# Kernel optimization log

Hardware: AMD Instinct MI355X
Metric: run time of the kernel (lower is better)

## Reference

```python
import jax, jax.numpy as jnp
import numpy as np

N, B, E, H, L, NF = 32768, 2048, 524288, 128, 7, 10
NODE_F = 60  # 10 frames * (loc 3 + vel 3)
OUT_F = 30   # 10 frames * 3


def _mlp(x, W1, b1, W2, b2):
    return jax.nn.relu(x @ W1 + b1) @ W2 + b2


def _lin(key, fan_in, fan_out):
    s = 1.0 / np.sqrt(fan_in)
    kw, kb = jax.random.split(key)
    W = jax.random.uniform(kw, (fan_in, fan_out), jnp.float32, -s, s)
    b = jax.random.uniform(kb, (fan_out,), jnp.float32, -s, s)
    return W, b


def setup_inputs() -> dict:
    key = jax.random.key(0)
    ks = jax.random.split(key, 12)
    p = {}
    p["loc"] = jax.random.normal(ks[0], (N, NF, 3), jnp.float32)
    p["vel"] = jax.random.normal(ks[1], (N, NF, 3), jnp.float32)
    p["y"] = jax.random.normal(ks[2], (N, NF, 3), jnp.float32)
    p["edge_index"] = jax.random.randint(ks[3], (2, E), 0, N, dtype=jnp.int64)
    p["batch_size"] = B
    # embedder: Linear(60,H) -> ReLU -> Linear(H,H)
    p["emb_W1"], p["emb_b1"] = _lin(ks[4], NODE_F, H)
    p["emb_W2"], p["emb_b2"] = _lin(ks[5], H, H)
    # per-layer message net Linear(2H,H)->ReLU->Linear(H,H); update net Linear(2H,H)->ReLU->Linear(H,H)
    mW1, mb1, mW2, mb2, uW1, ub1, uW2, ub2 = [], [], [], [], [], [], [], []
    for i in range(L):
        k = jax.random.fold_in(ks[6], i)
        k1, k2, k3, k4 = jax.random.split(k, 4)
        a, b = _lin(k1, 2 * H, H); mW1.append(a); mb1.append(b)
        a, b = _lin(k2, H, H); mW2.append(a); mb2.append(b)
        a, b = _lin(k3, 2 * H, H); uW1.append(a); ub1.append(b)
        a, b = _lin(k4, H, H); uW2.append(a); ub2.append(b)
    p["msg_W1"] = jnp.stack(mW1); p["msg_b1"] = jnp.stack(mb1)
    p["msg_W2"] = jnp.stack(mW2); p["msg_b2"] = jnp.stack(mb2)
    p["upd_W1"] = jnp.stack(uW1); p["upd_b1"] = jnp.stack(ub1)
    p["upd_W2"] = jnp.stack(uW2); p["upd_b2"] = jnp.stack(ub2)
    # head: Linear(H,H) -> ReLU -> Linear(H,30)
    p["head_W1"], p["head_b1"] = _lin(ks[7], H, H)
    p["head_W2"], p["head_b2"] = _lin(ks[8], H, OUT_F)
    return p


def reference(loc, vel, y, edge_index, batch_size,
              emb_W1, emb_b1, emb_W2, emb_b2,
              msg_W1, msg_b1, msg_W2, msg_b2,
              upd_W1, upd_b1, upd_W2, upd_b2,
              head_W1, head_b1, head_W2, head_b2):
    n = loc.shape[0]
    src, dst = edge_index[0], edge_index[1]  # x_j = x[src], x_i = x[dst] (PyG source_to_target)
    x = jnp.concatenate([loc, vel], axis=-1).reshape(n, -1)  # (N, 60)
    x = _mlp(x, emb_W1, emb_b1, emb_W2, emb_b2)              # (N, H)
    for i in range(L):
        m_in = jnp.concatenate([x[dst], x[src]], axis=-1)    # (E, 2H) cat(x_i, x_j)
        msg = _mlp(m_in, msg_W1[i], msg_b1[i], msg_W2[i], msg_b2[i])  # (E, H)
        agg = jax.ops.segment_sum(msg, dst, num_segments=n)  # scatter-add at targets
        x = _mlp(jnp.concatenate([x, agg], axis=-1), upd_W1[i], upd_b1[i], upd_W2[i], upd_b2[i])
    x = _mlp(x, head_W1, head_b1, head_W2, head_b2)          # (N, 30)
    loc_pred = x.reshape(n, NF, 3) + loc
    d = jnp.sqrt(jnp.sum((loc_pred - y) ** 2, axis=-1))      # (N, NF)
    ade_loss = d.reshape(batch_size, -1, NF).mean(axis=-1).mean(axis=-1)  # (B,)
    fde = jnp.sqrt(jnp.sum((loc_pred[:, -1, :] - y[:, -1, :]) ** 2, axis=-1))  # (N,)
    fde_loss = fde.reshape(batch_size, -1).mean(axis=-1)     # (B,)
    backprop_loss = ade_loss.mean()
    return backprop_loss, ade_loss, fde_loss
```

## Files before the change

### kernel.cpp

```cpp
#include <hip/hip_runtime.h>
#include <hip/hip_bf16.h>
#include <stdint.h>

#define HH 128

typedef __attribute__((ext_vector_type(8))) short short8;
typedef __attribute__((ext_vector_type(4))) float floatx4;

typedef __attribute__((address_space(3))) uint32_t lds_u32_t;
typedef const __attribute__((address_space(1))) uint32_t gbl_u32_t;

__device__ __forceinline__ void gl_lds16(const void* g, void* l) {
  __builtin_amdgcn_global_load_lds((gbl_u32_t*)g, (lds_u32_t*)l, 16, 0, 0);
}

__device__ __forceinline__ float bf2f(short v) {
  union { uint32_t u; float f; } x; x.u = ((uint32_t)(uint16_t)v) << 16; return x.f;
}
__device__ __forceinline__ short f2bf(float f) {
  union { float f; uint32_t u; } x; x.f = f;
  uint32_t r = x.u + 0x7fffu + ((x.u >> 16) & 1u);
  return (short)(r >> 16);
}
__device__ __forceinline__ float rdf(const void* p, int i, int fl) {
  return fl ? bf2f(((const short*)p)[i]) : ((const float*)p)[i];
}


__global__ void detect_zero(const int* __restrict__ eidx, int* iflag, int* dflag,
                            int* __restrict__ counts, float* accp,
                            const uint32_t* __restrict__ loc, int N) {
  int g = blockIdx.x * 256 + threadIdx.x;
  if (g < N) counts[g] = 0;
  if (blockIdx.x == 0) {
    __shared__ int nz, cnt;
    if (threadIdx.x == 0) { nz = 0; cnt = 0; *accp = 0.f; }
    __syncthreads();
    int any = 0;
    for (int i = threadIdx.x; i < 1024; i += 256) any |= (eidx[2 * i + 1] != 0);
    if (any) atomicOr(&nz, 1);
    uint32_t u = loc[threadIdx.x];
    int e = (u >> 7) & 0xFF;
    if (e >= 100 && e <= 140) atomicAdd(&cnt, 1);
    __syncthreads();
    if (threadIdx.x == 0) {
      *iflag = (nz == 0) ? 1 : 0;
      *dflag = (cnt >= 192) ? 1 : 0;
    }
  }
}


__global__ void pad_input(const void* __restrict__ loc, const void* __restrict__ vel,
                          short* __restrict__ dst, const int* __restrict__ dflag) {
  int fl = *dflag;
  int idx = blockIdx.x * 256 + threadIdx.x;
  int j = idx & 63, i = idx >> 6;
  short v = 0;
  if (j < 60) {
    int f = j / 6, c = j % 6;
    float x = (c < 3) ? rdf(loc, (i * 10 + f) * 3 + c, fl)
                      : rdf(vel, (i * 10 + f) * 3 + (c - 3), fl);
    v = f2bf(x);
  }
  dst[idx] = v;
}

struct WPrep {
  const void* src[8];
// ... 97 lines not shown
  int x = c;
#pragma unroll
  for (int off = 1; off < 64; off <<= 1) {
    int u = __shfl_up(x, off);
    if (lane >= off) x += u;
  }
  if (lane == 63) wsum[w] = x;
  __syncthreads();
  int wpre = 0;
#pragma unroll
  for (int k = 0; k < 4; ++k)
    if (k < w) wpre += wsum[k];
  int excl = shb[0] + shb[1] + wpre + x - c;
  if (i < N) {
    row_start[i] = excl;
    cursor[i] = excl;
    deg[i] = (float)c;
  }
  if (i == N - 1) row_start[N] = E;
}

__global__ void scatter_kernel(const int* __restrict__ eidx, const int* __restrict__ iflag,
                               int* __restrict__ cursor, int* __restrict__ ssrc, int E) {
  int e = blockIdx.x * 256 + threadIdx.x;
  if (e >= E) return;
  int fl = *iflag;
  int d = fl ? eidx[2 * (E + e)] : eidx[E + e];
  int sv = fl ? eidx[2 * e] : eidx[e];
  int pos = atomicAdd(&cursor[d], 1);
  ssrc[pos] = sv;
}


__global__ __launch_bounds__(256)
void edge_agg(const uint32_t* __restrict__ Pp, const uint32_t* __restrict__ Qp,
              const int* __restrict__ ssrc, const int* __restrict__ row_start,
              uint32_t* __restrict__ Hagg, int Ntot) {
  int w = threadIdx.x >> 6, lane = threadIdx.x & 63;
  int d = blockIdx.x * 4 + w;
  if (d >= Ntot) return;
  uint32_t pv = Pp[(size_t)d * 64 + lane];
  float px = bf2f((short)(pv & 0xffff));
  float py = bf2f((short)(pv >> 16));
  int s0 = row_start[d], s1 = row_start[d + 1];
  float ax = 0.f, ay = 0.f;
  int e = s0;
  for (; e + 8 <= s1; e += 8) {
    int idx[8];
    uint32_t q[8];
#pragma unroll
    for (int u = 0; u < 8; ++u) idx[u] = ssrc[e + u];
#pragma unroll
    for (int u = 0; u < 8; ++u) q[u] = Qp[(size_t)idx[u] * 64 + lane];
#pragma unroll
    for (int u = 0; u < 8; ++u) {
      float hx = px + bf2f((short)(q[u] & 0xffff));
      float hy = py + bf2f((short)(q[u] >> 16));
      ax += hx > 0.f ? hx : 0.f;
      ay += hy > 0.f ? hy : 0.f;
    }
  }
  for (; e < s1; ++e) {
    int i0 = ssrc[e];
    uint32_t q0 = Qp[(size_t)i0 * 64 + lane];
    float hx = px + bf2f((short)(q0 & 0xffff));
    float hy = py + bf2f((short)(q0 >> 16));
    ax += hx > 0.f ? hx : 0.f;
    ay += hy > 0.f ? hy : 0.f;
  }
  uint32_t packed = (uint32_t)(uint16_t)f2bf(ax) | ((uint32_t)(uint16_t)f2bf(ay) << 16);
  Hagg[(size_t)d * 64 + lane] = packed;
}


__device__ __forceinline__ void write_aslots_q(char* lds, const floatx4 v[2][4],
                                               int wr, int wc, int quad, int l16) {
#pragma unroll
  for (int mt = 0; mt < 2; ++mt) {
    int g = wr * 2 + mt;
#pragma unroll
    for (int nt = 0; nt < 4; ++nt) {
      int s2 = wc * 2 + (nt >> 1);
      int qc = (nt & 1) * 2 + (l16 >> 3);
      char* base = lds + (size_t)(s2 * 8 + g) * 1024 + 2 * (l16 & 7);
#pragma unroll
      for (int r = 0; r < 4; ++r)
        *(short*)(base + (quad * 4 + r + 16 * qc) * 16) = f2bf(v[mt][nt][r]);
    }
  }
}

template <int NT, int TS>
__device__ __forceinline__ void gemm_q(const char* lds, int wr, int wc,
                                       floatx4 acc[2][NT], int lane) {
#pragma unroll
  for (int s2 = 0; s2 < 4; ++s2) {
    short8 af[2];
#pragma unroll
    for (int mt = 0; mt < 2; ++mt)
      af[mt] = *(const short8*)(lds + (s2 * 8 + wr * 2 + mt) * 1024 + lane * 16);
    short8 bf[NT];
#pragma unroll
    for (int nt = 0; nt < NT; ++nt)
      bf[nt] = *(const short8*)(lds + 32768 + (s2 * TS + wc * NT + nt) * 1024 + lane * 16);
#pragma unroll
    for (int mt = 0; mt < 2; ++mt)
#pragma unroll
      for (int nt = 0; nt < NT; ++nt)
        acc[mt][nt] = __builtin_amdgcn_mfma_f32_16x16x32_bf16(af[mt], bf[nt], acc[mt][nt], 0, 0, 0);
  }
}


template <int MODE>
__global__ __launch_bounds__(512, 2)
void mlp_fused(const short* __restrict__ Asrc, const short* __restrict__ Asrc2,
               const short* __restrict__ W1T, const float* __restrict__ b1,
               const short* __restrict__ W2T, const float* __restrict__ b2,
               const float* __restrict__ deg, const float* __restrict__ b2Uv,
               const short* __restrict__ pqW1, const float* __restrict__ pqB1,
               const short* __restrict__ pq2W, const float* __restrict__ pq2B,
               short* __restrict__ xout, short* __restrict__ Pout,
               short* __restrict__ Qout, float* __restrict__ out32) {
  constexpr int K1 = (MODE == 0) ? 64 : 256;
  constexpr int NS = K1 / 32;
  constexpr int PQS = (MODE == 3) ? 128 : 256;

  __shared__ __align__(16) char lds[65536];

  const int tid = threadIdx.x;
  const int w = tid >> 6, lane = tid & 63;
  const int quad = lane >> 4, l16 = lane & 15;
  const int wr = w >> 1, wc = w & 1;
  const int R0 = blockIdx.x * 128;
  const int CB = wc * 64;

#pragma unroll
  for (int c = 0; c < NS; ++c) {
    int slot = w * NS + c;
    int s = slot >> 3, t = slot & 7;
    int n = t * 16 + l16, k = s * 32 + quad * 8;
    gl_lds16(W1T + n * K1 + k, lds + slot * 1024 + lane * 16);
  }

  short8 afrag[NS][2];
  if constexpr (MODE == 0) {
#pragma unroll
    for (int mt = 0; mt < 2; ++mt) {
      int m = R0 + wr * 32 + mt * 16 + l16;
      const short* pr = Asrc + (size_t)m * 64;
#pragma unroll
      for (int s = 0; s < NS; ++s) afrag[s][mt] = *(const short8*)(pr + s * 32 + quad * 8);
    }
  } else {
#pragma unroll
    for (int mt = 0; mt < 2; ++mt) {
      int m = R0 + wr * 32 + mt * 16 + l16;
      const short* pr = Asrc + (size_t)m * HH;
      const short* ar = Asrc2 + (size_t)m * HH;
#pragma unroll
      for (int s = 0; s < 4; ++s) {
        afrag[s][mt] = *(const short8*)(pr + s * 32 + quad * 8);
        afrag[s + 4][mt] = *(const short8*)(ar + s * 32 + quad * 8);
      }
    }
  }

  float b1f[4], b2f[4], pb1[4], b2u[4];
  float dvals[2][4];
#pragma unroll
  for (int t = 0; t < 4; ++t) {
    int col = CB + t * 16 + l16;
    b1f[t] = b1[col];
    b2f[t] = b2[col];
    pb1[t] = pqB1[col];
  }
  if constexpr (MODE != 0) {
#pragma unroll
    for (int t = 0; t < 4; ++t) b2u[t] = b2Uv[CB + t * 16 + l16];
#pragma unroll
    for (int mt = 0; mt < 2; ++mt)
#pragma unroll
      for (int r = 0; r < 4; ++r)
        dvals[mt][r] = deg[R0 + wr * 32 + mt * 16 + quad * 4 + r];
  }

  __syncthreads();

  floatx4 zero4 = {0.f, 0.f, 0.f, 0.f};
  floatx4 acc[2][4];
#pragma unroll
  for (int mt = 0; mt < 2; ++mt)
#pragma unroll
    for (int t = 0; t < 4; ++t) acc[mt][t] = zero4;
#pragma unroll
  for (int s = 0; s < NS; ++s) {
    short8 bfrag[4];
#pragma unroll
    for (int nt = 0; nt < 4; ++nt)
      bfrag[nt] = *(const short8*)(lds + (s * 8 + wc * 4 + nt) * 1024 + lane * 16);
#pragma unroll
    for (int mt = 0; mt < 2; ++mt)
#pragma unroll
      for (int nt = 0; nt < 4; ++nt)
        acc[mt][nt] = __builtin_amdgcn_mfma_f32_16x16x32_bf16(afrag[s][mt], bfrag[nt], acc[mt][nt], 0, 0, 0);
  }

  __syncthreads();

#pragma unroll
  for (int c = 0; c < 4; ++c) {
    int slot = w * 4 + c;
    int s2 = slot >> 3, t = slot & 7;
    int n = t * 16 + l16, k = s2 * 32 + quad * 8;
    gl_lds16(W2T + n * HH + k, lds + 32768 + slot * 1024 + lane * 16);
  }
  {
    floatx4 hv[2][4];
#pragma unroll
    for (int mt = 0; mt < 2; ++mt)
#pragma unroll
      for (int nt = 0; nt < 4; ++nt)
#pragma unroll
        for (int r = 0; r < 4; ++r) {
          float h = acc[mt][nt][r] + b1f[nt];
          if constexpr (MODE != 0) h += dvals[mt][r] * b2u[nt];
          hv[mt][nt][r] = h > 0.f ? h : 0.f;
        }
    write_aslots_q(lds, hv, wr, wc, quad, l16);
  }

  __syncthreads();

  floatx4 acc2[2][4];
#pragma unroll
  for (int mt = 0; mt < 2; ++mt)
#pragma unroll
    for (int t = 0; t < 4; ++t) acc2[mt][t] = zero4;
  gemm_q<4, 8>(lds, wr, wc, acc2, lane);

  floatx4 xv[2][4];
#pragma unroll
  for (int mt = 0; mt < 2; ++mt)
#pragma unroll
    for (int nt = 0; nt < 4; ++nt)
#pragma unroll
      for (int r = 0; r < 4; ++r)
        xv[mt][nt][r] = acc2[mt][nt][r] + b2f[nt];

  if constexpr (MODE != 3) {
#pragma unroll
    for (int mt = 0; mt < 2; ++mt)
#pragma unroll
      for (int nt = 0; nt < 4; ++nt) {
        int col = CB + nt * 16 + l16;
#pragma unroll
        for (int r = 0; r < 4; ++r) {
          int row = R0 + wr * 32 + mt * 16 + quad * 4 + r;
          xout[(size_t)row * HH + col] = f2bf(xv[mt][nt][r]);
        }
      }
  }

  __syncthreads();

  write_aslots_q(lds, xv, wr, wc, quad, l16);
#pragma unroll
  for (int c = 0; c < 4; ++c) {
    int slot = w * 4 + c;
    int s2 = slot >> 3, t = slot & 7;
    int n = t * 16 + l16, k = s2 * 32 + quad * 8;
    gl_lds16(pqW1 + n * PQS + k, lds + 32768 + slot * 1024 + lane * 16);
  }

  __syncthreads();

  floatx4 accc[2][4];
#pragma unroll
  for (int mt = 0; mt < 2; ++mt)
#pragma unroll
    for (int t = 0; t < 4; ++t) accc[mt][t] = zero4;
  gemm_q<4, 8>(lds, wr, wc, accc, lane);

  if constexpr (MODE == 3) {
    floatx4 h2[2][4];
#pragma unroll
    for (int mt = 0; mt < 2; ++mt)
#pragma unroll
      for (int nt = 0; nt < 4; ++nt)
#pragma unroll
        for (int r = 0; r < 4; ++r) {
          float h = accc[mt][nt][r] + pb1[nt];
          h2[mt][nt][r] = h > 0.f ? h : 0.f;
        }
    __syncthreads();
    write_aslots_q(lds, h2, wr, wc, quad, l16);
    {
      int s2 = w >> 1, t = w & 1;
      int n = t * 16 + l16, k = s2 * 32 + quad * 8;
      gl_lds16(pq2W + n * 128 + k, lds + 32768 + w * 1024 + lane * 16);
    }
    __syncthreads();
    floatx4 acco[2][1];
#pragma unroll
    for (int mt = 0; mt < 2; ++mt) acco[mt][0] = zero4;
    gemm_q<1, 2>(lds, wr, wc, acco, lane);
    float ob = pq2B[wc * 16 + l16];
#pragma unroll
    for (int mt = 0; mt < 2; ++mt) {
      int col = wc * 16 + l16;
#pragma unroll
      for (int r = 0; r < 4; ++r) {
        int row = R0 + wr * 32 + mt * 16 + quad * 4 + r;
        out32[(size_t)row * 32 + col] = acco[mt][0][r] + ob;
      }
    }
  } else {
#pragma unroll
    for (int mt = 0; mt < 2; ++mt)
#pragma unroll
      for (int nt = 0; nt < 4; ++nt) {
        int col = CB + nt * 16 + l16;
#pragma unroll
        for (int r = 0; r < 4; ++r) {
          int row = R0 + wr * 32 + mt * 16 + quad * 4 + r;
          Pout[(size_t)row * HH + col] = f2bf(accc[mt][nt][r] + pb1[nt]);
        }
      }
    __syncthreads();
#pragma unroll
    for (int c = 0; c < 4; ++c) {
      int slot = w * 4 + c;
      int s2 = slot >> 3, t = slot & 7;
      int n = t * 16 + l16, k = s2 * 32 + quad * 8;
      gl_lds16(pqW1 + n * 256 + 128 + k, lds + 32768 + slot * 1024 + lane * 16);
    }
    __syncthreads();
    floatx4 accq[2][4];
#pragma unroll
    for (int mt = 0; mt < 2; ++mt)
#pragma unroll
      for (int t = 0; t < 4; ++t) accq[mt][t] = zero4;
    gemm_q<4, 8>(lds, wr, wc, accq, lane);
#pragma unroll
    for (int mt = 0; mt < 2; ++mt)
#pragma unroll
      for (int nt = 0; nt < 4; ++nt) {
        int col = CB + nt * 16 + l16;
#pragma unroll
        for (int r = 0; r < 4; ++r) {
          int row = R0 + wr * 32 + mt * 16 + quad * 4 + r;
          Qout[(size_t)row * HH + col] = f2bf(accq[mt][nt][r]);
        }
      }
  }
}


__global__ void loss_kernel(const float* __restrict__ out32, const void* __restrict__ loc,
                            const void* __restrict__ yv, const int* __restrict__ dflag,
                            float* __restrict__ out, float* __restrict__ acc, int NB) {
  int fl = *dflag;
  int i = blockIdx.x * 256 + threadIdx.x;
  const float* o = out32 + (size_t)i * 32;
  float dsum = 0.f, fde = 0.f;
#pragma unroll
  for (int f = 0; f < 10; ++f) {
    float dx = o[f * 3 + 0] + rdf(loc, i * 30 + f * 3 + 0, fl) - rdf(yv, i * 30 + f * 3 + 0, fl);
    float dy = o[f * 3 + 1] + rdf(loc, i * 30 + f * 3 + 1, fl) - rdf(yv, i * 30 + f * 3 + 1, fl);
    float dz = o[f * 3 + 2] + rdf(loc, i * 30 + f * 3 + 2, fl) - rdf(yv, i * 30 + f * 3 + 2, fl);
    float d = sqrtf(dx * dx + dy * dy + dz * dz);
    dsum += d;
    if (f == 9) fde = d;
  }
#pragma unroll
  for (int m = 1; m < 16; m <<= 1) {
    dsum += __shfl_xor(dsum, m);
    fde += __shfl_xor(fde, m);
  }
  if ((threadIdx.x & 15) == 0) {
    int b = i >> 4;
    out[1 + b] = dsum / 160.0f;
    out[1 + NB + b] = fde / 16.0f;
    unsafeAtomicAdd(acc, dsum);
  }
}

__global__ void final_kernel(const float* __restrict__ acc, float* __restrict__ out, float inv) {
  if (threadIdx.x == 0) out[0] = *acc * inv;
}


extern "C" void kernel_launch(void* const* d_in, const int* in_sizes, int n_in,
                              void* d_out, int out_size, void* d_ws, size_t ws_size,
                              hipStream_t stream) {
  const void* loc = d_in[0];
  const void* vel = d_in[1];
  const void* yv = d_in[2];
  const int* eidx = (const int*)d_in[3];

  const int N = in_sizes[0] / 30;
  const int E = in_sizes[3] / 2;
  const int L = 7;
  const int NB = N / 16;

  const size_t MB = 1024 * 1024;
  char* ws = (char*)d_ws;
  short* x = (short*)ws;
  short* P = (short*)(ws + 8 * MB);
  short* Qs = (short*)(ws + 24 * MB);
  short* Hagg = (short*)(ws + 32 * MB);
  short* updW1Tf = (short*)(ws + 40 * MB);
  int* bsums = (int*)(ws + 41 * MB);
  short* wbase = (short*)(ws + 48 * MB);
  const unsigned long long OFF_EMBW1 = 0;
  const unsigned long long OFF_EMBW2 = 8192;
  const unsigned long long OFF_HEADW1 = 24576;
  const unsigned long long OFF_HEADW2 = 40960;
  const unsigned long long OFF_MSGW1 = 45056;
  const unsigned long long OFF_MSGW2 = 274432;
  const unsigned long long OFF_UPDW1 = 389120;
  const unsigned long long OFF_UPDW2 = 618496;
  short* embW1T = wbase + OFF_EMBW1;
  short* embW2T = wbase + OFF_EMBW2;
  short* headW1T = wbase + OFF_HEADW1;
  short* headW2T = wbase + OFF_HEADW2;
  short* msgW1T = wbase + OFF_MSGW1;
  short* msgW2T = wbase + OFF_MSGW2;
  short* updW1T = wbase + OFF_UPDW1;
  short* updW2T = wbase + OFF_UPDW2;
  float* bias = (float*)(ws + 49 * MB + 512 * 1024);
  float* embB1f = bias;
  float* embB2f = bias + 128;
  float* msgB1f = bias + 256;
  float* msgB2f = bias + 1152;
  float* updB1f = bias + 2048;
  float* updB2f = bias + 2944;
  float* headB1f = bias + 3840;
  float* headB2f = bias + 3968;
  float* b2U = bias + 4096;
  int* counts = (int*)(ws + 49 * MB + 768 * 1024);
  int* row_start = (int*)(ws + 50 * MB);
  int* cursor = (int*)(ws + 50 * MB + 256 * 1024);
  float* deg = (float*)(ws + 50 * MB + 512 * 1024);
  int* iflag = (int*)(ws + 50 * MB + 768 * 1024);
  int* dflag = iflag + 16;
  float* accp = (float*)(iflag + 32);
  int* ssrc = (int*)(ws + 51 * MB);
  short* in64 = (short*)(ws + 53 * MB);
  float* out32 = (float*)(ws + 57 * MB);

  const int NBLK = (N + 255) / 256;

  detect_zero<<<NBLK, 256, 0, stream>>>(eidx, iflag, dflag, counts, accp,
                                        (const uint32_t*)loc, N);
  hist_kernel<<<(E + 255) / 256, 256, 0, stream>>>(eidx, iflag, counts, E);
  scan_bsum<<<NBLK, 256, 0, stream>>>(counts, bsums, N);
  scan_final<<<NBLK, 256, 0, stream>>>(counts, bsums, row_start, cursor, deg, N, E);
  scatter_kernel<<<(E + 255) / 256, 256, 0, stream>>>(eidx, iflag, cursor, ssrc, E);

  pad_input<<<(N * 64) / 256, 256, 0, stream>>>(loc, vel, in64, dflag);

  {
    WPrep a;
    const void* srcs[8] = {d_in[5], d_in[7], d_in[17], d_in[19],
                           d_in[9], d_in[11], d_in[13], d_in[15]};
    unsigned long long offs[8] = {OFF_EMBW1, OFF_EMBW2, OFF_HEADW1, OFF_HEADW2,
                                  OFF_MSGW1, OFF_MSGW2, OFF_UPDW1, OFF_UPDW2};
    int Ls[8] = {1, 1, 1, 1, 7, 7, 7, 7};
    int Ks[8] = {60, 128, 128, 128, 256, 128, 256, 128};
    int Ns[8] = {128, 128, 128, 30, 128, 128, 128, 128};
    int Kps[8] = {64, 128, 128, 128, 256, 128, 256, 128};
    int Nps[8] = {128, 128, 128, 32, 128, 128, 128, 128};
    int cum = 0;
    for (int s = 0; s < 8; ++s) {
      a.src[s] = srcs[s]; a.dstoff[s] = offs[s];
      a.L[s] = Ls[s]; a.K[s] = Ks[s]; a.Nn[s] = Ns[s]; a.Kp[s] = Kps[s]; a.Np[s] = Nps[s];
      a.bstart[s] = cum;
      cum += (Ls[s] * Nps[s] * Kps[s] + 255) / 256;
    }
    a.bstart[8] = cum;
    prep_w<<<cum, 256, 0, stream>>>(a, wbase, dflag);
  }
  {
    BPrep a;
    const void* srcs[8] = {d_in[6], d_in[8], d_in[10], d_in[12],
                           d_in[14], d_in[16], d_in[18], d_in[20]};
    int ns[8] = {128, 128, 896, 896, 896, 896, 128, 30};
    int es[9] = {0, 128, 256, 1152, 2048, 2944, 3840, 3968, 4000};
    for (int s = 0; s < 8; ++s) { a.src[s] = srcs[s]; a.n[s] = ns[s]; a.estart[s] = es[s]; }
    a.estart[8] = es[8];
    prep_b<<<16, 256, 0, stream>>>(a, bias, dflag);
  }

  fold_kernel<<<900, 256, 0, stream>>>(updW1T, msgW2T, updW1Tf, msgB2f, b2U);

  mlp_fused<0><<<N / 128, 512, 0, stream>>>(in64, nullptr,
      embW1T, embB1f, embW2T, embB2f, nullptr, nullptr,
      msgW1T, msgB1f, nullptr, nullptr, x, P, Qs, nullptr);

  for (int l = 0; l < L; ++l) {
    edge_agg<<<(N + 3) / 4, 256, 0, stream>>>((const uint32_t*)P, (const uint32_t*)Qs,
                                              ssrc, row_start, (uint32_t*)Hagg, N);
    if (l < L - 1) {
      mlp_fused<2><<<N / 128, 512, 0, stream>>>(x, Hagg,
          updW1Tf + l * 128 * 256, updB1f + l * 128, updW2T + l * 128 * 128, updB2f + l * 128,
          deg, b2U + l * 128,
          msgW1T + (l + 1) * 128 * 256, msgB1f + (l + 1) * 128, nullptr, nullptr,
          x, P, Qs, nullptr);
    } else {
      mlp_fused<3><<<N / 128, 512, 0, stream>>>(x, Hagg,
          updW1Tf + l * 128 * 256, updB1f + l * 128, updW2T + l * 128 * 128, updB2f + l * 128,
          deg, b2U + l * 128,
          headW1T, headB1f, headW2T, headB2f,
          nullptr, nullptr, nullptr, out32);
    }
  }

  loss_kernel<<<N / 256, 256, 0, stream>>>(out32, loc, yv, dflag, (float*)d_out, accp, NB);
  final_kernel<<<1, 64, 0, stream>>>(accp, (float*)d_out, 1.0f / 327680.0f);
}
```

Baseline: 531.4 us.

## Shrink fused MLP tiles to 32 rows with 2 waves and unroll edge tail

The fused node MLP kernel now processes 32 rows per block with 128 threads (2 waves) instead of 128 rows with 512 threads. This launches 4x more blocks and uses a smaller 40KB LDS footprint, so more blocks can be resident and the grid fills the device more evenly. In exchange, each block reloads the full weight matrices, and the K=256 first layer is split into two staged halves, which adds syncs and weight traffic per row. Separately, the edge aggregation remainder loop is replaced by 4/2/1 unrolled tails so more gathers are in flight at once.

```diff
diff --git a/kernel.cpp b/kernel.cpp
--- a/kernel.cpp
+++ b/kernel.cpp
@@ -212,8 +212,7 @@
   float ax = 0.f, ay = 0.f;
   int e = s0;
   for (; e + 8 <= s1; e += 8) {
-    int idx[8];
-    uint32_t q[8];
+    int idx[8]; uint32_t q[8];
 #pragma unroll
     for (int u = 0; u < 8; ++u) idx[u] = ssrc[e + u];
 #pragma unroll
@@ -226,7 +225,32 @@
       ay += hy > 0.f ? hy : 0.f;
     }
   }
-  for (; e < s1; ++e) {
+  if (e + 4 <= s1) {
+    int idx[4]; uint32_t q[4];
+#pragma unroll
+    for (int u = 0; u < 4; ++u) idx[u] = ssrc[e + u];
+#pragma unroll
+    for (int u = 0; u < 4; ++u) q[u] = Qp[(size_t)idx[u] * 64 + lane];
+#pragma unroll
+    for (int u = 0; u < 4; ++u) {
+      float hx = px + bf2f((short)(q[u] & 0xffff));
+      float hy = py + bf2f((short)(q[u] >> 16));
+      ax += hx > 0.f ? hx : 0.f;
+      ay += hy > 0.f ? hy : 0.f;
+    }
+    e += 4;
+  }
+  if (e + 2 <= s1) {
+    int i0 = ssrc[e], i1 = ssrc[e + 1];
+    uint32_t q0 = Qp[(size_t)i0 * 64 + lane];
+    uint32_t q1 = Qp[(size_t)i1 * 64 + lane];
+    float hx = px + bf2f((short)(q0 & 0xffff)), hy = py + bf2f((short)(q0 >> 16));
+    ax += hx > 0.f ? hx : 0.f; ay += hy > 0.f ? hy : 0.f;
+    hx = px + bf2f((short)(q1 & 0xffff)); hy = py + bf2f((short)(q1 >> 16));
+    ax += hx > 0.f ? hx : 0.f; ay += hy > 0.f ? hy : 0.f;
+    e += 2;
+  }
+  if (e < s1) {
     int i0 = ssrc[e];
     uint32_t q0 = Qp[(size_t)i0 * 64 + lane];
     float hx = px + bf2f((short)(q0 & 0xffff));
@@ -239,36 +263,34 @@
 }
 
 
-__device__ __forceinline__ void write_aslots_q(char* lds, const floatx4 v[2][4],
-                                               int wr, int wc, int quad, int l16) {
-#pragma unroll
-  for (int mt = 0; mt < 2; ++mt) {
-    int g = wr * 2 + mt;
+__device__ __forceinline__ void write_aslots32(char* lds, const floatx4 v[2][4],
+                                               int wc, int quad, int l16) {
+#pragma unroll
+  for (int mt = 0; mt < 2; ++mt)
 #pragma unroll
     for (int nt = 0; nt < 4; ++nt) {
       int s2 = wc * 2 + (nt >> 1);
       int qc = (nt & 1) * 2 + (l16 >> 3);
-      char* base = lds + (size_t)(s2 * 8 + g) * 1024 + 2 * (l16 & 7);
+      char* base = lds + (size_t)(s2 * 2 + mt) * 1024 + 2 * (l16 & 7);
 #pragma unroll
       for (int r = 0; r < 4; ++r)
         *(short*)(base + (quad * 4 + r + 16 * qc) * 16) = f2bf(v[mt][nt][r]);
     }
-  }
 }
 
 template <int NT, int TS>
-__device__ __forceinline__ void gemm_q(const char* lds, int wr, int wc,
-                                       floatx4 acc[2][NT], int lane) {
+__device__ __forceinline__ void gemm32(const char* lds, int wc, floatx4 acc[2][NT], int lane) {
+  const char* ldsB = lds + 8192;
 #pragma unroll
   for (int s2 = 0; s2 < 4; ++s2) {
     short8 af[2];
 #pragma unroll
     for (int mt = 0; mt < 2; ++mt)
-      af[mt] = *(const short8*)(lds + (s2 * 8 + wr * 2 + mt) * 1024 + lane * 16);
+      af[mt] = *(const short8*)(lds + (s2 * 2 + mt) * 1024 + lane * 16);
     short8 bf[NT];
 #pragma unroll
     for (int nt = 0; nt < NT; ++nt)
-      bf[nt] = *(const short8*)(lds + 32768 + (s2 * TS + wc * NT + nt) * 1024 + lane * 16);
+      bf[nt] = *(const short8*)(ldsB + (s2 * TS + wc * NT + nt) * 1024 + lane * 16);
 #pragma unroll
     for (int mt = 0; mt < 2; ++mt)
 #pragma unroll
@@ -279,7 +301,7 @@
 
 
 template <int MODE>
-__global__ __launch_bounds__(512, 2)
+__global__ __launch_bounds__(128, 2)
 void mlp_fused(const short* __restrict__ Asrc, const short* __restrict__ Asrc2,
                const short* __restrict__ W1T, const float* __restrict__ b1,
                const short* __restrict__ W2T, const float* __restrict__ b2,
@@ -289,39 +311,49 @@
                short* __restrict__ xout, short* __restrict__ Pout,
                short* __restrict__ Qout, float* __restrict__ out32) {
   constexpr int K1 = (MODE == 0) ? 64 : 256;
-  constexpr int NS = K1 / 32;
+  constexpr int NSA = K1 / 32;
   constexpr int PQS = (MODE == 3) ? 128 : 256;
 
-  __shared__ __align__(16) char lds[65536];
+  __shared__ __align__(16) char lds[40960];
+  char* ldsB = lds + 8192;
 
   const int tid = threadIdx.x;
-  const int w = tid >> 6, lane = tid & 63;
+  const int wc = tid >> 6, lane = tid & 63;
   const int quad = lane >> 4, l16 = lane & 15;
-  const int wr = w >> 1, wc = w & 1;
-  const int R0 = blockIdx.x * 128;
+  const int R0 = blockIdx.x * 32;
   const int CB = wc * 64;
 
-#pragma unroll
-  for (int c = 0; c < NS; ++c) {
-    int slot = w * NS + c;
-    int s = slot >> 3, t = slot & 7;
-    int n = t * 16 + l16, k = s * 32 + quad * 8;
-    gl_lds16(W1T + n * K1 + k, lds + slot * 1024 + lane * 16);
-  }
-
-  short8 afrag[NS][2];
   if constexpr (MODE == 0) {
 #pragma unroll
+    for (int c = 0; c < 8; ++c) {
+      int slot = wc * 8 + c;
+      int s = slot >> 3, t = slot & 7;
+      gl_lds16(W1T + (t * 16 + l16) * 64 + s * 32 + quad * 8,
+               ldsB + slot * 1024 + lane * 16);
+    }
+  } else {
+#pragma unroll
+    for (int c = 0; c < 16; ++c) {
+      int slot = wc * 16 + c;
+      int s2 = slot >> 3, t = slot & 7;
+      gl_lds16(W1T + (t * 16 + l16) * 256 + s2 * 32 + quad * 8,
+               ldsB + slot * 1024 + lane * 16);
+    }
+  }
+
+  short8 afrag[NSA][2];
+  if constexpr (MODE == 0) {
+#pragma unroll
     for (int mt = 0; mt < 2; ++mt) {
-      int m = R0 + wr * 32 + mt * 16 + l16;
+      int m = R0 + mt * 16 + l16;
       const short* pr = Asrc + (size_t)m * 64;
 #pragma unroll
-      for (int s = 0; s < NS; ++s) afrag[s][mt] = *(const short8*)(pr + s * 32 + quad * 8);
+      for (int s = 0; s < 2; ++s) afrag[s][mt] = *(const short8*)(pr + s * 32 + quad * 8);
     }
   } else {
 #pragma unroll
     for (int mt = 0; mt < 2; ++mt) {
-      int m = R0 + wr * 32 + mt * 16 + l16;
+      int m = R0 + mt * 16 + l16;
       const short* pr = Asrc + (size_t)m * HH;
       const short* ar = Asrc2 + (size_t)m * HH;
 #pragma unroll
@@ -348,7 +380,7 @@
     for (int mt = 0; mt < 2; ++mt)
 #pragma unroll
       for (int r = 0; r < 4; ++r)
-        dvals[mt][r] = deg[R0 + wr * 32 + mt * 16 + quad * 4 + r];
+        dvals[mt][r] = deg[R0 + mt * 16 + quad * 4 + r];
   }
 
   __syncthreads();
@@ -359,27 +391,54 @@
   for (int mt = 0; mt < 2; ++mt)
 #pragma unroll
     for (int t = 0; t < 4; ++t) acc[mt][t] = zero4;
-#pragma unroll
-  for (int s = 0; s < NS; ++s) {
-    short8 bfrag[4];
-#pragma unroll
-    for (int nt = 0; nt < 4; ++nt)
-      bfrag[nt] = *(const short8*)(lds + (s * 8 + wc * 4 + nt) * 1024 + lane * 16);
-#pragma unroll
-    for (int mt = 0; mt < 2; ++mt)
+  {
+    constexpr int NS0 = (MODE == 0) ? 2 : 4;
+#pragma unroll
+    for (int s = 0; s < NS0; ++s) {
+      short8 bfrag[4];
 #pragma unroll
       for (int nt = 0; nt < 4; ++nt)
-        acc[mt][nt] = __builtin_amdgcn_mfma_f32_16x16x32_bf16(afrag[s][mt], bfrag[nt], acc[mt][nt], 0, 0, 0);
+        bfrag[nt] = *(const short8*)(ldsB + (s * 8 + wc * 4 + nt) * 1024 + lane * 16);
+#pragma unroll
+      for (int mt = 0; mt < 2; ++mt)
+#pragma unroll
+        for (int nt = 0; nt < 4; ++nt)
+          acc[mt][nt] = __builtin_amdgcn_mfma_f32_16x16x32_bf16(afrag[s][mt], bfrag[nt], acc[mt][nt], 0, 0, 0);
+    }
+  }
+
+  if constexpr (MODE != 0) {
+    __syncthreads();
+#pragma unroll
+    for (int c = 0; c < 16; ++c) {
+      int slot = wc * 16 + c;
+      int s2 = slot >> 3, t = slot & 7;
+      gl_lds16(W1T + (t * 16 + l16) * 256 + 128 + s2 * 32 + quad * 8,
+               ldsB + slot * 1024 + lane * 16);
+    }
+    __syncthreads();
+#pragma unroll
+    for (int s = 0; s < 4; ++s) {
+      short8 bfrag[4];
+#pragma unroll
+      for (int nt = 0; nt < 4; ++nt)
+        bfrag[nt] = *(const short8*)(ldsB + (s * 8 + wc * 4 + nt) * 1024 + lane * 16);
+#pragma unroll
+      for (int mt = 0; mt < 2; ++mt)
+#pragma unroll
+        for (int nt = 0; nt < 4; ++nt)
+          acc[mt][nt] = __builtin_amdgcn_mfma_f32_16x16x32_bf16(afrag[4 + s][mt], bfrag[nt], acc[mt][nt], 0, 0, 0);
+    }
   }
 
   __syncthreads();
 
 #pragma unroll
-  for (int c = 0; c < 4; ++c) {
-    int slot = w * 4 + c;
+  for (int c = 0; c < 16; ++c) {
+    int slot = wc * 16 + c;
     int s2 = slot >> 3, t = slot & 7;
-    int n = t * 16 + l16, k = s2 * 32 + quad * 8;
-    gl_lds16(W2T + n * HH + k, lds + 32768 + slot * 1024 + lane * 16);
+    gl_lds16(W2T + (t * 16 + l16) * HH + s2 * 32 + quad * 8,
+             ldsB + slot * 1024 + lane * 16);
   }
   {
     floatx4 hv[2][4];
@@ -393,7 +452,7 @@
           if constexpr (MODE != 0) h += dvals[mt][r] * b2u[nt];
           hv[mt][nt][r] = h > 0.f ? h : 0.f;
         }
-    write_aslots_q(lds, hv, wr, wc, quad, l16);
+    write_aslots32(lds, hv, wc, quad, l16);
   }
 
   __syncthreads();
@@ -403,7 +462,7 @@
   for (int mt = 0; mt < 2; ++mt)
 #pragma unroll
     for (int t = 0; t < 4; ++t) acc2[mt][t] = zero4;
-  gemm_q<4, 8>(lds, wr, wc, acc2, lane);
+  gemm32<4, 8>(lds, wc, acc2, lane);
 
   floatx4 xv[2][4];
 #pragma unroll
@@ -422,7 +481,7 @@
         int col = CB + nt * 16 + l16;
 #pragma unroll
         for (int r = 0; r < 4; ++r) {
-          int row = R0 + wr * 32 + mt * 16 + quad * 4 + r;
+          int row = R0 + mt * 16 + quad * 4 + r;
           xout[(size_t)row * HH + col] = f2bf(xv[mt][nt][r]);
         }
       }
@@ -430,13 +489,13 @@
 
   __syncthreads();
 
-  write_aslots_q(lds, xv, wr, wc, quad, l16);
-#pragma unroll
-  for (int c = 0; c < 4; ++c) {
-    int slot = w * 4 + c;
+  write_aslots32(lds, xv, wc, quad, l16);
+#pragma unroll
+  for (int c = 0; c < 16; ++c) {
+    int slot = wc * 16 + c;
     int s2 = slot >> 3, t = slot & 7;
-    int n = t * 16 + l16, k = s2 * 32 + quad * 8;
-    gl_lds16(pqW1 + n * PQS + k, lds + 32768 + slot * 1024 + lane * 16);
+    gl_lds16(pqW1 + (t * 16 + l16) * PQS + s2 * 32 + quad * 8,
+             ldsB + slot * 1024 + lane * 16);
   }
 
   __syncthreads();
@@ -446,7 +505,7 @@
   for (int mt = 0; mt < 2; ++mt)
 #pragma unroll
     for (int t = 0; t < 4; ++t) accc[mt][t] = zero4;
-  gemm_q<4, 8>(lds, wr, wc, accc, lane);
+  gemm32<4, 8>(lds, wc, accc, lane);
 
   if constexpr (MODE == 3) {
     floatx4 h2[2][4];
@@ -460,24 +519,26 @@
           h2[mt][nt][r] = h > 0.f ? h : 0.f;
         }
     __syncthreads();
-    write_aslots_q(lds, h2, wr, wc, quad, l16);
-    {
-      int s2 = w >> 1, t = w & 1;
-      int n = t * 16 + l16, k = s2 * 32 + quad * 8;
-      gl_lds16(pq2W + n * 128 + k, lds + 32768 + w * 1024 + lane * 16);
+    write_aslots32(lds, h2, wc, quad, l16);
+#pragma unroll
+    for (int c = 0; c < 4; ++c) {
+      int slot = wc * 4 + c;
+      int s2 = slot >> 1, t = slot & 1;
+      gl_lds16(pq2W + (t * 16 + l16) * 128 + s2 * 32 + quad * 8,
+               ldsB + slot * 1024 + lane * 16);
     }
     __syncthreads();
     floatx4 acco[2][1];
 #pragma unroll
     for (int mt = 0; mt < 2; ++mt) acco[mt][0] = zero4;
-    gemm_q<1, 2>(lds, wr, wc, acco, lane);
+    gemm32<1, 2>(lds, wc, acco, lane);
     float ob = pq2B[wc * 16 + l16];
 #pragma unroll
     for (int mt = 0; mt < 2; ++mt) {
       int col = wc * 16 + l16;
 #pragma unroll
       for (int r = 0; r < 4; ++r) {
-        int row = R0 + wr * 32 + mt * 16 + quad * 4 + r;
+        int row = R0 + mt * 16 + quad * 4 + r;
         out32[(size_t)row * 32 + col] = acco[mt][0][r] + ob;
       }
     }
@@ -489,17 +550,17 @@
         int col = CB + nt * 16 + l16;
 #pragma unroll
         for (int r = 0; r < 4; ++r) {
-          int row = R0 + wr * 32 + mt * 16 + quad * 4 + r;
+          int row = R0 + mt * 16 + quad * 4 + r;
           Pout[(size_t)row * HH + col] = f2bf(accc[mt][nt][r] + pb1[nt]);
         }
       }
     __syncthreads();
 #pragma unroll
-    for (int c = 0; c < 4; ++c) {
-      int slot = w * 4 + c;
+    for (int c = 0; c < 16; ++c) {
+      int slot = wc * 16 + c;
       int s2 = slot >> 3, t = slot & 7;
-      int n = t * 16 + l16, k = s2 * 32 + quad * 8;
-      gl_lds16(pqW1 + n * 256 + 128 + k, lds + 32768 + slot * 1024 + lane * 16);
+      gl_lds16(pqW1 + (t * 16 + l16) * 256 + 128 + s2 * 32 + quad * 8,
+               ldsB + slot * 1024 + lane * 16);
     }
     __syncthreads();
     floatx4 accq[2][4];
@@ -507,7 +568,7 @@
     for (int mt = 0; mt < 2; ++mt)
 #pragma unroll
       for (int t = 0; t < 4; ++t) accq[mt][t] = zero4;
-    gemm_q<4, 8>(lds, wr, wc, accq, lane);
+    gemm32<4, 8>(lds, wc, accq, lane);
 #pragma unroll
     for (int mt = 0; mt < 2; ++mt)
 #pragma unroll
@@ -515,7 +576,7 @@
         int col = CB + nt * 16 + l16;
 #pragma unroll
         for (int r = 0; r < 4; ++r) {
-          int row = R0 + wr * 32 + mt * 16 + quad * 4 + r;
+          int row = R0 + mt * 16 + quad * 4 + r;
           Qout[(size_t)row * HH + col] = f2bf(accq[mt][nt][r]);
         }
       }
@@ -661,7 +722,7 @@
 
   fold_kernel<<<900, 256, 0, stream>>>(updW1T, msgW2T, updW1Tf, msgB2f, b2U);
 
-  mlp_fused<0><<<N / 128, 512, 0, stream>>>(in64, nullptr,
+  mlp_fused<0><<<N / 32, 128, 0, stream>>>(in64, nullptr,
       embW1T, embB1f, embW2T, embB2f, nullptr, nullptr,
       msgW1T, msgB1f, nullptr, nullptr, x, P, Qs, nullptr);
 
@@ -669,13 +730,13 @@
     edge_agg<<<(N + 3) / 4, 256, 0, stream>>>((const uint32_t*)P, (const uint32_t*)Qs,
                                               ssrc, row_start, (uint32_t*)Hagg, N);
     if (l < L - 1) {
-      mlp_fused<2><<<N / 128, 512, 0, stream>>>(x, Hagg,
+      mlp_fused<2><<<N / 32, 128, 0, stream>>>(x, Hagg,
           updW1Tf + l * 128 * 256, updB1f + l * 128, updW2T + l * 128 * 128, updB2f + l * 128,
           deg, b2U + l * 128,
           msgW1T + (l + 1) * 128 * 256, msgB1f + (l + 1) * 128, nullptr, nullptr,
           x, P, Qs, nullptr);
     } else {
-      mlp_fused<3><<<N / 128, 512, 0, stream>>>(x, Hagg,
+      mlp_fused<3><<<N / 32, 128, 0, stream>>>(x, Hagg,
           updW1Tf + l * 128 * 256, updB1f + l * 128, updW2T + l * 128 * 128, updB2f + l * 128,
           deg, b2U + l * 128,
           headW1T, headB1f, headW2T, headB2f,
```

After: 567.8 us. +6.8%, slower.

## Fuse edge aggregation gather into update MLP kernel and drop final kernel

Applied to the files above, without the earlier changes.

Edge aggregation (gather of Q rows by CSR plus ReLU-sum) now runs inside the update MLP kernel and writes the aggregate straight into swizzled LDS, so the Hagg round trip through global memory and one launch per layer go away. P/Q are double-buffered because the same kernel reads the previous layer's values and writes the next layer's. The final scalar reduction is folded into the loss kernel with a last-block ticket counter. The cost is that the irregular gather now runs inside a kernel with 512-thread blocks at 2 blocks per CU, so it may hide gather latency less well than the dedicated kernel did.

```diff
diff --git a/kernel.cpp b/kernel.cpp
--- a/kernel.cpp
+++ b/kernel.cpp
@@ -28,13 +28,13 @@
 
 
 __global__ void detect_zero(const int* __restrict__ eidx, int* iflag, int* dflag,
-                            int* __restrict__ counts, float* accp,
+                            int* __restrict__ counts, float* accp, int* ticket,
                             const uint32_t* __restrict__ loc, int N) {
   int g = blockIdx.x * 256 + threadIdx.x;
   if (g < N) counts[g] = 0;
   if (blockIdx.x == 0) {
     __shared__ int nz, cnt;
-    if (threadIdx.x == 0) { nz = 0; cnt = 0; *accp = 0.f; }
+    if (threadIdx.x == 0) { nz = 0; cnt = 0; *accp = 0.f; *ticket = 0; }
     __syncthreads();
     int any = 0;
     for (int i = threadIdx.x; i < 1024; i += 256) any |= (eidx[2 * i + 1] != 0);
@@ -198,47 +198,6 @@
 }
 
 
-__global__ __launch_bounds__(256)
-void edge_agg(const uint32_t* __restrict__ Pp, const uint32_t* __restrict__ Qp,
-              const int* __restrict__ ssrc, const int* __restrict__ row_start,
-              uint32_t* __restrict__ Hagg, int Ntot) {
-  int w = threadIdx.x >> 6, lane = threadIdx.x & 63;
-  int d = blockIdx.x * 4 + w;
-  if (d >= Ntot) return;
-  uint32_t pv = Pp[(size_t)d * 64 + lane];
-  float px = bf2f((short)(pv & 0xffff));
-  float py = bf2f((short)(pv >> 16));
-  int s0 = row_start[d], s1 = row_start[d + 1];
-  float ax = 0.f, ay = 0.f;
-  int e = s0;
-  for (; e + 8 <= s1; e += 8) {
-    int idx[8];
-    uint32_t q[8];
-#pragma unroll
-    for (int u = 0; u < 8; ++u) idx[u] = ssrc[e + u];
-#pragma unroll
-    for (int u = 0; u < 8; ++u) q[u] = Qp[(size_t)idx[u] * 64 + lane];
-#pragma unroll
-    for (int u = 0; u < 8; ++u) {
-      float hx = px + bf2f((short)(q[u] & 0xffff));
-      float hy = py + bf2f((short)(q[u] >> 16));
-      ax += hx > 0.f ? hx : 0.f;
-      ay += hy > 0.f ? hy : 0.f;
-    }
-  }
-  for (; e < s1; ++e) {
-    int i0 = ssrc[e];
-    uint32_t q0 = Qp[(size_t)i0 * 64 + lane];
-    float hx = px + bf2f((short)(q0 & 0xffff));
-    float hy = py + bf2f((short)(q0 >> 16));
-    ax += hx > 0.f ? hx : 0.f;
-    ay += hy > 0.f ? hy : 0.f;
-  }
-  uint32_t packed = (uint32_t)(uint16_t)f2bf(ax) | ((uint32_t)(uint16_t)f2bf(ay) << 16);
-  Hagg[(size_t)d * 64 + lane] = packed;
-}
-
-
 __device__ __forceinline__ void write_aslots_q(char* lds, const floatx4 v[2][4],
                                                int wr, int wc, int quad, int l16) {
 #pragma unroll
@@ -280,7 +239,9 @@
 
 template <int MODE>
 __global__ __launch_bounds__(512, 2)
-void mlp_fused(const short* __restrict__ Asrc, const short* __restrict__ Asrc2,
+void mlp_fused(const short* __restrict__ Asrc,
+               const uint32_t* __restrict__ Pp, const uint32_t* __restrict__ Qp,
+               const int* __restrict__ ssrc, const int* __restrict__ row_start,
                const short* __restrict__ W1T, const float* __restrict__ b1,
                const short* __restrict__ W2T, const float* __restrict__ b2,
                const float* __restrict__ deg, const float* __restrict__ b2Uv,
@@ -288,11 +249,10 @@
                const short* __restrict__ pq2W, const float* __restrict__ pq2B,
                short* __restrict__ xout, short* __restrict__ Pout,
                short* __restrict__ Qout, float* __restrict__ out32) {
-  constexpr int K1 = (MODE == 0) ? 64 : 256;
-  constexpr int NS = K1 / 32;
   constexpr int PQS = (MODE == 3) ? 128 : 256;
 
   __shared__ __align__(16) char lds[65536];
+  char* HB = lds + 32768;
 
   const int tid = threadIdx.x;
   const int w = tid >> 6, lane = tid & 63;
@@ -301,37 +261,6 @@
   const int R0 = blockIdx.x * 128;
   const int CB = wc * 64;
 
-#pragma unroll
-  for (int c = 0; c < NS; ++c) {
-    int slot = w * NS + c;
-    int s = slot >> 3, t = slot & 7;
-    int n = t * 16 + l16, k = s * 32 + quad * 8;
-    gl_lds16(W1T + n * K1 + k, lds + slot * 1024 + lane * 16);
-  }
-
-  short8 afrag[NS][2];
-  if constexpr (MODE == 0) {
-#pragma unroll
-    for (int mt = 0; mt < 2; ++mt) {
-      int m = R0 + wr * 32 + mt * 16 + l16;
-      const short* pr = Asrc + (size_t)m * 64;
-#pragma unroll
-      for (int s = 0; s < NS; ++s) afrag[s][mt] = *(const short8*)(pr + s * 32 + quad * 8);
-    }
-  } else {
-#pragma unroll
-    for (int mt = 0; mt < 2; ++mt) {
-      int m = R0 + wr * 32 + mt * 16 + l16;
-      const short* pr = Asrc + (size_t)m * HH;
-      const short* ar = Asrc2 + (size_t)m * HH;
-#pragma unroll
-      for (int s = 0; s < 4; ++s) {
-        afrag[s][mt] = *(const short8*)(pr + s * 32 + quad * 8);
-        afrag[s + 4][mt] = *(const short8*)(ar + s * 32 + quad * 8);
-      }
-    }
-  }
-
   float b1f[4], b2f[4], pb1[4], b2u[4];
   float dvals[2][4];
 #pragma unroll
@@ -341,7 +270,66 @@
     b2f[t] = b2[col];
     pb1[t] = pqB1[col];
   }
-  if constexpr (MODE != 0) {
+
+  short8 afrag[4][2];
+  floatx4 zero4 = {0.f, 0.f, 0.f, 0.f};
+  floatx4 acc[2][4];
+#pragma unroll
+  for (int mt = 0; mt < 2; ++mt)
+#pragma unroll
+    for (int t = 0; t < 4; ++t) acc[mt][t] = zero4;
+
+  if constexpr (MODE == 0) {
+#pragma unroll
+    for (int c = 0; c < 2; ++c) {
+      int slot = w * 2 + c;
+      int s = slot >> 3, t = slot & 7;
+      gl_lds16(W1T + (t * 16 + l16) * 64 + s * 32 + quad * 8,
+               lds + slot * 1024 + lane * 16);
+    }
+#pragma unroll
+    for (int mt = 0; mt < 2; ++mt) {
+      int m = R0 + wr * 32 + mt * 16 + l16;
+      const short* pr = Asrc + (size_t)m * 64;
+#pragma unroll
+      for (int s = 0; s < 2; ++s) afrag[s][mt] = *(const short8*)(pr + s * 32 + quad * 8);
+    }
+    __syncthreads();
+#pragma unroll
+    for (int s = 0; s < 2; ++s) {
+      short8 bfrag[4];
+#pragma unroll
+      for (int nt = 0; nt < 4; ++nt)
+        bfrag[nt] = *(const short8*)(lds + (s * 8 + wc * 4 + nt) * 1024 + lane * 16);
+#pragma unroll
+      for (int mt = 0; mt < 2; ++mt)
+#pragma unroll
+        for (int nt = 0; nt < 4; ++nt)
+          acc[mt][nt] = __builtin_amdgcn_mfma_f32_16x16x32_bf16(afrag[s][mt], bfrag[nt], acc[mt][nt], 0, 0, 0);
+    }
+    __syncthreads();
+#pragma unroll
+    for (int c = 0; c < 4; ++c) {
+      int slot = w * 4 + c;
+      int s2 = slot >> 3, t = slot & 7;
+      gl_lds16(W2T + (t * 16 + l16) * HH + s2 * 32 + quad * 8,
+               HB + slot * 1024 + lane * 16);
+    }
+  } else {
+#pragma unroll
+    for (int c = 0; c < 4; ++c) {
+      int slot = w * 4 + c;
+      int s = slot >> 3, t = slot & 7;
+      gl_lds16(W1T + (t * 16 + l16) * 256 + s * 32 + quad * 8,
+               lds + slot * 1024 + lane * 16);
+    }
+#pragma unroll
+    for (int mt = 0; mt < 2; ++mt) {
+      int m = R0 + wr * 32 + mt * 16 + l16;
+      const short* pr = Asrc + (size_t)m * HH;
+#pragma unroll
+      for (int s = 0; s < 4; ++s) afrag[s][mt] = *(const short8*)(pr + s * 32 + quad * 8);
+    }
 #pragma unroll
     for (int t = 0; t < 4; ++t) b2u[t] = b2Uv[CB + t * 16 + l16];
 #pragma unroll
@@ -349,38 +337,111 @@
 #pragma unroll
       for (int r = 0; r < 4; ++r)
         dvals[mt][r] = deg[R0 + wr * 32 + mt * 16 + quad * 4 + r];
-  }
-
-  __syncthreads();
-
-  floatx4 zero4 = {0.f, 0.f, 0.f, 0.f};
-  floatx4 acc[2][4];
-#pragma unroll
-  for (int mt = 0; mt < 2; ++mt)
-#pragma unroll
-    for (int t = 0; t < 4; ++t) acc[mt][t] = zero4;
-#pragma unroll
-  for (int s = 0; s < NS; ++s) {
-    short8 bfrag[4];
-#pragma unroll
-    for (int nt = 0; nt < 4; ++nt)
-      bfrag[nt] = *(const short8*)(lds + (s * 8 + wc * 4 + nt) * 1024 + lane * 16);
-#pragma unroll
-    for (int mt = 0; mt < 2; ++mt)
+
+    for (int i = 0; i < 16; ++i) {
+      int mr = w * 16 + i;
+      int d = R0 + mr;
+      uint32_t pv = Pp[(size_t)d * 64 + lane];
+      float px = bf2f((short)(pv & 0xffff));
+      float py = bf2f((short)(pv >> 16));
+      int s0 = row_start[d], s1 = row_start[d + 1];
+      float ax = 0.f, ay = 0.f;
+      int e = s0;
+      for (; e + 8 <= s1; e += 8) {
+        int idx[8]; uint32_t q[8];
+#pragma unroll
+        for (int u = 0; u < 8; ++u) idx[u] = ssrc[e + u];
+#pragma unroll
+        for (int u = 0; u < 8; ++u) q[u] = Qp[(size_t)idx[u] * 64 + lane];
+#pragma unroll
+        for (int u = 0; u < 8; ++u) {
+          float hx = px + bf2f((short)(q[u] & 0xffff));
+          float hy = py + bf2f((short)(q[u] >> 16));
+          ax += hx > 0.f ? hx : 0.f;
+          ay += hy > 0.f ? hy : 0.f;
+        }
+      }
+      if (e + 4 <= s1) {
+        int idx[4]; uint32_t q[4];
+#pragma unroll
+        for (int u = 0; u < 4; ++u) idx[u] = ssrc[e + u];
+#pragma unroll
+        for (int u = 0; u < 4; ++u) q[u] = Qp[(size_t)idx[u] * 64 + lane];
+#pragma unroll
+        for (int u = 0; u < 4; ++u) {
+          float hx = px + bf2f((short)(q[u] & 0xffff));
+          float hy = py + bf2f((short)(q[u] >> 16));
+          ax += hx > 0.f ? hx : 0.f;
+          ay += hy > 0.f ? hy : 0.f;
+        }
+        e += 4;
+      }
+      for (; e < s1; ++e) {
+        int i0 = ssrc[e];
+        uint32_t q0 = Qp[(size_t)i0 * 64 + lane];
+        float hx = px + bf2f((short)(q0 & 0xffff));
+        float hy = py + bf2f((short)(q0 >> 16));
+        ax += hx > 0.f ? hx : 0.f;
+        ay += hy > 0.f ? hy : 0.f;
+      }
+      uint32_t packed = (uint32_t)(uint16_t)f2bf(ax) | ((uint32_t)(uint16_t)f2bf(ay) << 16);
+      *(uint32_t*)(HB + mr * 256 + (((lane >> 2) ^ i) << 4) + ((lane & 3) << 2)) = packed;
+    }
+    __syncthreads();
+
+    short8 hfrag[4][2];
+#pragma unroll
+    for (int mt = 0; mt < 2; ++mt) {
+      int mr = (wr * 2 + mt) * 16 + l16;
+#pragma unroll
+      for (int s = 0; s < 4; ++s)
+        hfrag[s][mt] = *(const short8*)(HB + mr * 256 + (((s * 4 + quad) ^ l16) << 4));
+    }
+#pragma unroll
+    for (int s = 0; s < 4; ++s) {
+      short8 bfrag[4];
 #pragma unroll
       for (int nt = 0; nt < 4; ++nt)
-        acc[mt][nt] = __builtin_amdgcn_mfma_f32_16x16x32_bf16(afrag[s][mt], bfrag[nt], acc[mt][nt], 0, 0, 0);
-  }
-
-  __syncthreads();
-
-#pragma unroll
-  for (int c = 0; c < 4; ++c) {
-    int slot = w * 4 + c;
-    int s2 = slot >> 3, t = slot & 7;
-    int n = t * 16 + l16, k = s2 * 32 + quad * 8;
-    gl_lds16(W2T + n * HH + k, lds + 32768 + slot * 1024 + lane * 16);
-  }
+        bfrag[nt] = *(const short8*)(lds + (s * 8 + wc * 4 + nt) * 1024 + lane * 16);
+#pragma unroll
+      for (int mt = 0; mt < 2; ++mt)
+#pragma unroll
+        for (int nt = 0; nt < 4; ++nt)
+          acc[mt][nt] = __builtin_amdgcn_mfma_f32_16x16x32_bf16(afrag[s][mt], bfrag[nt], acc[mt][nt], 0, 0, 0);
+    }
+    __syncthreads();
+
+#pragma unroll
+    for (int c = 0; c < 4; ++c) {
+      int slot = w * 4 + c;
+      int s = slot >> 3, t = slot & 7;
+      gl_lds16(W1T + (t * 16 + l16) * 256 + 128 + s * 32 + quad * 8,
+               lds + slot * 1024 + lane * 16);
+    }
+#pragma unroll
+    for (int c = 0; c < 4; ++c) {
+      int slot = w * 4 + c;
+      int s2 = slot >> 3, t = slot & 7;
+      gl_lds16(W2T + (t * 16 + l16) * HH + s2 * 32 + quad * 8,
+               HB + slot * 1024 + lane * 16);
+    }
+    __syncthreads();
+
+#pragma unroll
+    for (int s = 0; s < 4; ++s) {
+      short8 bfrag[4];
+#pragma unroll
+      for (int nt = 0; nt < 4; ++nt)
+        bfrag[nt] = *(const short8*)(lds + (s * 8 + wc * 4 + nt) * 1024 + lane * 16);
+#pragma unroll
+      for (int mt = 0; mt < 2; ++mt)
+#pragma unroll
+        for (int nt = 0; nt < 4; ++nt)
+          acc[mt][nt] = __builtin_amdgcn_mfma_f32_16x16x32_bf16(hfrag[s][mt], bfrag[nt], acc[mt][nt], 0, 0, 0);
+    }
+    __syncthreads();
+  }
+
   {
     floatx4 hv[2][4];
 #pragma unroll
@@ -395,7 +456,6 @@
         }
     write_aslots_q(lds, hv, wr, wc, quad, l16);
   }
-
   __syncthreads();
 
   floatx4 acc2[2][4];
@@ -427,7 +487,6 @@
         }
       }
   }
-
   __syncthreads();
 
   write_aslots_q(lds, xv, wr, wc, quad, l16);
@@ -435,10 +494,9 @@
   for (int c = 0; c < 4; ++c) {
     int slot = w * 4 + c;
     int s2 = slot >> 3, t = slot & 7;
-    int n = t * 16 + l16, k = s2 * 32 + quad * 8;
-    gl_lds16(pqW1 + n * PQS + k, lds + 32768 + slot * 1024 + lane * 16);
-  }
-
+    gl_lds16(pqW1 + (t * 16 + l16) * PQS + s2 * 32 + quad * 8,
+             HB + slot * 1024 + lane * 16);
+  }
   __syncthreads();
 
   floatx4 accc[2][4];
@@ -463,8 +521,8 @@
     write_aslots_q(lds, h2, wr, wc, quad, l16);
     {
       int s2 = w >> 1, t = w & 1;
-      int n = t * 16 + l16, k = s2 * 32 + quad * 8;
-      gl_lds16(pq2W + n * 128 + k, lds + 32768 + w * 1024 + lane * 16);
+      gl_lds16(pq2W + (t * 16 + l16) * 128 + s2 * 32 + quad * 8,
+               HB + w * 1024 + lane * 16);
     }
     __syncthreads();
     floatx4 acco[2][1];
@@ -498,8 +556,8 @@
     for (int c = 0; c < 4; ++c) {
       int slot = w * 4 + c;
       int s2 = slot >> 3, t = slot & 7;
-      int n = t * 16 + l16, k = s2 * 32 + quad * 8;
-      gl_lds16(pqW1 + n * 256 + 128 + k, lds + 32768 + slot * 1024 + lane * 16);
+      gl_lds16(pqW1 + (t * 16 + l16) * 256 + 128 + s2 * 32 + quad * 8,
+               HB + slot * 1024 + lane * 16);
     }
     __syncthreads();
     floatx4 accq[2][4];
@@ -525,7 +583,8 @@
 
 __global__ void loss_kernel(const float* __restrict__ out32, const void* __restrict__ loc,
                             const void* __restrict__ yv, const int* __restrict__ dflag,
-                            float* __restrict__ out, float* __restrict__ acc, int NB) {
+                            float* __restrict__ out, float* __restrict__ acc,
+                            int* __restrict__ ticket, int NB, int nblocks, float inv) {
   int fl = *dflag;
   int i = blockIdx.x * 256 + threadIdx.x;
   const float* o = out32 + (size_t)i * 32;
@@ -550,10 +609,15 @@
     out[1 + NB + b] = fde / 16.0f;
     unsafeAtomicAdd(acc, dsum);
   }
-}
-
-__global__ void final_kernel(const float* __restrict__ acc, float* __restrict__ out, float inv) {
-  if (threadIdx.x == 0) out[0] = *acc * inv;
+  __threadfence();
+  __syncthreads();
+  if (threadIdx.x == 0) {
+    int old = atomicAdd(ticket, 1);
+    if (old == nblocks - 1) {
+      float v = unsafeAtomicAdd(acc, 0.0f);
+      out[0] = v * inv;
+    }
+  }
 }
 
 
@@ -573,9 +637,8 @@
   const size_t MB = 1024 * 1024;
   char* ws = (char*)d_ws;
   short* x = (short*)ws;
-  short* P = (short*)(ws + 8 * MB);
-  short* Qs = (short*)(ws + 24 * MB);
-  short* Hagg = (short*)(ws + 32 * MB);
+  short* Pb[2] = {(short*)(ws + 8 * MB), (short*)(ws + 16 * MB)};
+  short* Qb[2] = {(short*)(ws + 24 * MB), (short*)(ws + 32 * MB)};
   short* updW1Tf = (short*)(ws + 40 * MB);
   int* bsums = (int*)(ws + 41 * MB);
   short* wbase = (short*)(ws + 48 * MB);
@@ -612,13 +675,14 @@
   int* iflag = (int*)(ws + 50 * MB + 768 * 1024);
   int* dflag = iflag + 16;
   float* accp = (float*)(iflag + 32);
+  int* ticket = iflag + 48;
   int* ssrc = (int*)(ws + 51 * MB);
   short* in64 = (short*)(ws + 53 * MB);
   float* out32 = (float*)(ws + 57 * MB);
 
   const int NBLK = (N + 255) / 256;
 
-  detect_zero<<<NBLK, 256, 0, stream>>>(eidx, iflag, dflag, counts, accp,
+  detect_zero<<<NBLK, 256, 0, stream>>>(eidx, iflag, dflag, counts, accp, ticket,
                                         (const uint32_t*)loc, N);
   hist_kernel<<<(E + 255) / 256, 256, 0, stream>>>(eidx, iflag, counts, E);
   scan_bsum<<<NBLK, 256, 0, stream>>>(counts, bsums, N);
@@ -661,21 +725,22 @@
 
   fold_kernel<<<900, 256, 0, stream>>>(updW1T, msgW2T, updW1Tf, msgB2f, b2U);
 
-  mlp_fused<0><<<N / 128, 512, 0, stream>>>(in64, nullptr,
+  mlp_fused<0><<<N / 128, 512, 0, stream>>>(in64, nullptr, nullptr, nullptr, nullptr,
       embW1T, embB1f, embW2T, embB2f, nullptr, nullptr,
-      msgW1T, msgB1f, nullptr, nullptr, x, P, Qs, nullptr);
+      msgW1T, msgB1f, nullptr, nullptr, x, Pb[0], Qb[0], nullptr);
 
   for (int l = 0; l < L; ++l) {
-    edge_agg<<<(N + 3) / 4, 256, 0, stream>>>((const uint32_t*)P, (const uint32_t*)Qs,
-                                              ssrc, row_start, (uint32_t*)Hagg, N);
+    int pi = l & 1, po = (l + 1) & 1;
     if (l < L - 1) {
-      mlp_fused<2><<<N / 128, 512, 0, stream>>>(x, Hagg,
+      mlp_fused<2><<<N / 128, 512, 0, stream>>>(x,
+          (const uint32_t*)Pb[pi], (const uint32_t*)Qb[pi], ssrc, row_start,
           updW1Tf + l * 128 * 256, updB1f + l * 128, updW2T + l * 128 * 128, updB2f + l * 128,
           deg, b2U + l * 128,
           msgW1T + (l + 1) * 128 * 256, msgB1f + (l + 1) * 128, nullptr, nullptr,
-          x, P, Qs, nullptr);
+          x, Pb[po], Qb[po], nullptr);
     } else {
-      mlp_fused<3><<<N / 128, 512, 0, stream>>>(x, Hagg,
+      mlp_fused<3><<<N / 128, 512, 0, stream>>>(x,
+          (const uint32_t*)Pb[pi], (const uint32_t*)Qb[pi], ssrc, row_start,
           updW1Tf + l * 128 * 256, updB1f + l * 128, updW2T + l * 128 * 128, updB2f + l * 128,
           deg, b2U + l * 128,
           headW1T, headB1f, headW2T, headB2f,
@@ -683,6 +748,6 @@
     }
   }
 
-  loss_kernel<<<N / 256, 256, 0, stream>>>(out32, loc, yv, dflag, (float*)d_out, accp, NB);
-  final_kernel<<<1, 64, 0, stream>>>(accp, (float*)d_out, 1.0f / 327680.0f);
-}
+  loss_kernel<<<N / 256, 256, 0, stream>>>(out32, loc, yv, dflag, (float*)d_out, accp,
+                                           ticket, NB, N / 256, 1.0f / 327680.0f);
+}
```

After: 650.4 us. 1.22x slower.
